# Optimization experiments

Measured on AMD Instinct MI355X. Metric: run time of the kernel, lower is better.

## Reference

```python
import jax, jax.numpy as jnp
import numpy as np

N = 50000       # nodes
E = 800000      # edges (avg degree 16)
R = 8           # relations
IN = 128        # in_channels
H = 128         # hidden_size
B = 10          # graphs in batch
NPG = N // B    # nodes per graph (equal-size graphs)
NEG_SLOPE = 0.2 # RGATConv default negative_slope


def setup_inputs() -> dict:
    key = jax.random.key(0)
    ks = jax.random.split(key, 12)
    s = 0.1
    x = jax.random.normal(ks[0], (N, IN), dtype=jnp.float32)
    edge_index = jax.random.randint(ks[1], (2, E), 0, N, dtype=jnp.int32)
    edge_type = jax.random.randint(ks[2], (E,), 0, R, dtype=jnp.int32)
    batch = jnp.repeat(jnp.arange(B, dtype=jnp.int32), NPG)
    W1 = jax.random.normal(ks[3], (R, IN, H), dtype=jnp.float32) * s
    q1 = jax.random.normal(ks[4], (H, 1), dtype=jnp.float32) * s
    k1 = jax.random.normal(ks[5], (H, 1), dtype=jnp.float32) * s
    b1 = jnp.zeros((H,), dtype=jnp.float32)
    W2 = jax.random.normal(ks[6], (R, H, H), dtype=jnp.float32) * s
    q2 = jax.random.normal(ks[7], (H, 1), dtype=jnp.float32) * s
    k2 = jax.random.normal(ks[8], (H, 1), dtype=jnp.float32) * s
    b2 = jnp.zeros((H,), dtype=jnp.float32)
    Wl = jax.random.normal(ks[9], (H, H), dtype=jnp.float32) * s
    bl = jnp.zeros((H,), dtype=jnp.float32)
    return dict(x=x, edge_index=edge_index, edge_type=edge_type, batch=batch,
                W1=W1, q1=q1, k1=k1, b1=b1, W2=W2, q2=q2, k2=k2, b2=b2,
                Wl=Wl, bl=bl)


def _rgat_conv(x, src, tgt, etype, W, q, k, b):
    # Per-relation transform once per node ([R,N,H]), then gather per edge;
    # mathematically identical to PyG's per-edge bmm but avoids the [E,in,H] blowup.
    xW = jnp.einsum('ni,rio->rno', x, W)          # [R, N, H]
    outi = xW[etype, tgt]                          # [E, H] transformed target feats
    outj = xW[etype, src]                          # [E, H] transformed source feats
    # additive self-attention, heads=1, dim=1
    alpha = jax.nn.leaky_relu(outi @ q + outj @ k, NEG_SLOPE)  # [E, 1]
    # across-relation segment softmax over incoming edges of each target node
    m = jax.ops.segment_max(alpha, tgt, num_segments=N)        # [N, 1]
    a = jnp.exp(alpha - m[tgt])
    den = jax.ops.segment_sum(a, tgt, num_segments=N)          # [N, 1]
    a = a / (den[tgt] + 1e-16)
    out = jax.ops.segment_sum(a * outj, tgt, num_segments=N)   # [N, H]
    return out + b


def reference(x, edge_index, edge_type, batch, W1, q1, k1, b1,
              W2, q2, k2, b2, Wl, bl):
    src, tgt = edge_index[0], edge_index[1]
    h = jax.nn.relu(_rgat_conv(x, src, tgt, edge_type, W1, q1, k1, b1))
    # dropout p=0 -> identity
    h = jax.nn.relu(_rgat_conv(h, src, tgt, edge_type, W2, q2, k2, b2))
    h = h @ Wl.T + bl                               # nn.Linear
    # to_dense_batch: batch is sorted with equal-size graphs of NPG nodes
    return h.reshape(B, NPG, H)
```

## Files before the change

kernel.cpp:

```cpp
#include <hip/hip_runtime.h>


typedef unsigned int uint;
typedef unsigned short ushort_t;

using bf16x8 = __attribute__((ext_vector_type(8))) __bf16;
using f32x4  = __attribute__((ext_vector_type(4))) float;

__device__ __forceinline__ ushort_t fToBf(float f) {
  uint u = __float_as_uint(f);
  u += 0x7FFFu + ((u >> 16) & 1);
  return (ushort_t)(u >> 16);
}
__device__ __forceinline__ float bfToF(ushort_t h) {
  return __uint_as_float(((uint)h) << 16);
}


__global__ void k_count(const int* __restrict__ tgt, int* __restrict__ deg, int E) {
  int e = blockIdx.x * 256 + threadIdx.x;
  if (e < E) atomicAdd(&deg[tgt[e]], 1);
}

__global__ void k_scanA(const int* __restrict__ deg, int* __restrict__ incl,
                        int* __restrict__ bsum, int n) {
  __shared__ int s[256];
  int tid = threadIdx.x;
  int i = blockIdx.x * 256 + tid;
  int v = (i < n) ? deg[i] : 0;
  s[tid] = v;
  __syncthreads();
  for (int off = 1; off < 256; off <<= 1) {
    int t = (tid >= off) ? s[tid - off] : 0;
    __syncthreads();
    s[tid] += t;
    __syncthreads();
  }
  if (i < n) incl[i] = s[tid];
  if (tid == 255) bsum[blockIdx.x] = s[255];
}

__global__ void k_scanB(int* __restrict__ bsum, int nb) {
  __shared__ int s[256];
  int tid = threadIdx.x;
  int v = (tid < nb) ? bsum[tid] : 0;
  s[tid] = v;
  __syncthreads();
  for (int off = 1; off < 256; off <<= 1) {
    int t = (tid >= off) ? s[tid - off] : 0;
    __syncthreads();
    s[tid] += t;
    __syncthreads();
  }
  if (tid < nb) bsum[tid] = s[tid] - v;
}

__global__ void k_scanC(const int* __restrict__ deg, const int* __restrict__ incl,
                        const int* __restrict__ bsum, int* __restrict__ rowptr,
                        int n, int E) {
  int i = blockIdx.x * 256 + threadIdx.x;
  if (i < n) {
    rowptr[i] = bsum[blockIdx.x] + incl[i] - deg[i];
    if (i == n - 1) rowptr[n] = E;
  }
}

__global__ void k_scatter(const int* __restrict__ src, const int* __restrict__ tgt,
                          const int* __restrict__ et, const int* __restrict__ rowptr,
                          int* __restrict__ cursor, int* __restrict__ sorted, int E) {
  int e = blockIdx.x * 256 + threadIdx.x;
  if (e >= E) return;
  int t = tgt[e];
  int pos = atomicAdd(&cursor[t], 1);
  sorted[rowptr[t] + pos] = src[e] | (et[e] << 16);
}


__global__ void k_wT(const float* __restrict__ W1, const float* __restrict__ W2,
                     ushort_t* __restrict__ WT) {
  int b = blockIdx.x;
  const float* W = (b >= 1024) ? W2 : W1;
  int rn = b & 1023;
  int r = rn >> 7, n = rn & 127;
  int k = threadIdx.x;
  WT[(size_t)b * 128 + k] = fToBf(W[((size_t)r * 128 + k) * 128 + n]);
}

__global__ void k_wqwk(const float* __restrict__ W1, const float* __restrict__ q1,
                       const float* __restrict__ k1, const float* __restrict__ W2,
                       const float* __restrict__ q2, const float* __restrict__ k2,
                       ushort_t* __restrict__ wqk) {
  int g = blockIdx.x * 256 + threadIdx.x;
  if (g >= 4096) return;
  int layer = g >> 11;
  int which = (g >> 10) & 1;
  int idx = g & 1023;
  const float* w = (layer ? W2 : W1) + (size_t)idx * 128;
  const float* v = layer ? (which ? k2 : q2) : (which ? k1 : q1);
  float s = 0.f;
  #pragma unroll 8
  for (int h = 0; h < 128; h++) s += w[h] * v[h];
  int r = idx >> 7, kin = idx & 127;
  wqk[(size_t)layer * 2048 + ((which << 3) + r) * 128 + kin] = fToBf(s);
}


#define LDA 136

template <bool F32IN>
__global__ __launch_bounds__(256, 3) void
k_gemm8(const void* __restrict__ Ain, const ushort_t* __restrict__ WT,
        const ushort_t* __restrict__ Wqk, ushort_t* __restrict__ xW,
        float* __restrict__ stbl, int M) {
  __shared__ ushort_t rp[4][32 * LDA];
  int tid = threadIdx.x, wv = tid >> 6, lane = tid & 63;
  int l15 = lane & 15, quad = lane >> 4;
  int node0 = blockIdx.x * 128 + wv * 32;
  ushort_t* rpw = rp[wv];

  bf16x8 bx[2][4];
  #pragma unroll
  for (int nt = 0; nt < 2; nt++) {
    int node = node0 + nt * 16 + l15;
    if (node >= M) node = M - 1;
    if (F32IN) {
      const float* row = (const float*)Ain + (size_t)node * 128;
      #pragma unroll
      for (int kb = 0; kb < 4; kb++) {
        float4 a = *(const float4*)(row + kb * 32 + quad * 8);
        float4 b = *(const float4*)(row + kb * 32 + quad * 8 + 4);
        union { bf16x8 v; ushort_t u[8]; } t;
        t.u[0] = fToBf(a.x); t.u[1] = fToBf(a.y); t.u[2] = fToBf(a.z); t.u[3] = fToBf(a.w);
        t.u[4] = fToBf(b.x); t.u[5] = fToBf(b.y); t.u[6] = fToBf(b.z); t.u[7] = fToBf(b.w);
        bx[nt][kb] = t.v;
      }
    } else {
      const ushort_t* row = (const ushort_t*)Ain + (size_t)node * 128;
      #pragma unroll
      for (int kb = 0; kb < 4; kb++)
        bx[nt][kb] = *(const bf16x8*)(row + kb * 32 + quad * 8);
    }
  }

  for (int r = 0; r < 8; r++) {
    const ushort_t* Wr = WT + (size_t)r * 16384;
    f32x4 acc0[8] = {}, acc1[8] = {};
    #pragma unroll
    for (int mt = 0; mt < 8; mt++) {
      bf16x8 af[4];
      #pragma unroll
      for (int kb = 0; kb < 4; kb++)
        af[kb] = *(const bf16x8*)(Wr + (size_t)(mt * 16 + l15) * 128 + kb * 32 + quad * 8);
      #pragma unroll
      for (int kb = 0; kb < 4; kb++) {
        acc0[mt] = __builtin_amdgcn_mfma_f32_16x16x32_bf16(af[kb], bx[0][kb], acc0[mt], 0, 0, 0);
        acc1[mt] = __builtin_amdgcn_mfma_f32_16x16x32_bf16(af[kb], bx[1][kb], acc1[mt], 0, 0, 0);
      }
    }
    #pragma unroll
    for (int mt = 0; mt < 8; mt++) {
      uint2 p0, p1;
      p0.x = (uint)fToBf(acc0[mt][0]) | ((uint)fToBf(acc0[mt][1]) << 16);
      p0.y = (uint)fToBf(acc0[mt][2]) | ((uint)fToBf(acc0[mt][3]) << 16);
      p1.x = (uint)fToBf(acc1[mt][0]) | ((uint)fToBf(acc1[mt][1]) << 16);
      p1.y = (uint)fToBf(acc1[mt][2]) | ((uint)fToBf(acc1[mt][3]) << 16);
      *(uint2*)(rpw + (size_t)l15 * LDA + mt * 16 + quad * 4) = p0;
      *(uint2*)(rpw + (size_t)(16 + l15) * LDA + mt * 16 + quad * 4) = p1;
    }
    #pragma unroll
    for (int i = 0; i < 8; i++) {
      int row = i * 4 + quad;
      int off = l15 * 8;
      int node = node0 + row;
      if (node < M) {
        int4 v = *(const int4*)(rpw + (size_t)row * LDA + off);
        *(int4*)(xW + ((size_t)r * M + node) * 128 + off) = v;
      }
    }
  }

  bf16x8 aq[4];
  #pragma unroll
  for (int kb = 0; kb < 4; kb++)
    aq[kb] = *(const bf16x8*)(Wqk + (size_t)l15 * 128 + kb * 32 + quad * 8);
  #pragma unroll
  for (int nt = 0; nt < 2; nt++) {
    f32x4 acc = {};
    #pragma unroll
    for (int kb = 0; kb < 4; kb++)
      acc = __builtin_amdgcn_mfma_f32_16x16x32_bf16(aq[kb], bx[nt][kb], acc, 0, 0, 0);
    int node = node0 + nt * 16 + l15;
    if (node < M) *(float4*)(stbl + (size_t)node * 16 + quad * 4) = *(float4*)&acc;
  }
}

__global__ __launch_bounds__(256) void
k_gemmL(const ushort_t* __restrict__ A, const float* __restrict__ Wl,
        float* __restrict__ Cout, const float* __restrict__ bias, int M) {
  __shared__ ushort_t As[64 * LDA];
  __shared__ ushort_t Bs[128 * LDA];
  int tid = threadIdx.x;
  int row0 = blockIdx.x * 64;
  for (int c = tid; c < 1024; c += 256) {
    int r = c >> 4, off = (c & 15) * 8;
    int4 v = {0, 0, 0, 0};
    if (row0 + r < M) v = *(const int4*)(A + (size_t)(row0 + r) * 128 + off);
    *(int4*)(As + r * LDA + off) = v;
  }
  for (int c = tid; c < 2048; c += 256) {
    int nn = c >> 4, off = (c & 15) * 8;
    float4 a = *(const float4*)(Wl + (size_t)nn * 128 + off);
    float4 b = *(const float4*)(Wl + (size_t)nn * 128 + off + 4);
    ushort_t* d = Bs + nn * LDA + off;
    d[0] = fToBf(a.x); d[1] = fToBf(a.y); d[2] = fToBf(a.z); d[3] = fToBf(a.w);
    d[4] = fToBf(b.x); d[5] = fToBf(b.y); d[6] = fToBf(b.z); d[7] = fToBf(b.w);
  }
  __syncthreads();
  int wv = tid >> 6, lane = tid & 63;
  int l15 = lane & 15, quad = lane >> 4;
  int wr = wv * 16;
  bf16x8 afr[4];
  #pragma unroll
  for (int kb = 0; kb < 4; kb++)
    afr[kb] = *reinterpret_cast<const bf16x8*>(As + (wr + l15) * LDA + kb * 32 + quad * 8);
  f32x4 acc[8] = {};
  #pragma unroll
  for (int ct = 0; ct < 8; ct++)
    #pragma unroll
    for (int kb = 0; kb < 4; kb++) {
      bf16x8 bfr = *reinterpret_cast<const bf16x8*>(Bs + (ct * 16 + l15) * LDA + kb * 32 + quad * 8);
      acc[ct] = __builtin_amdgcn_mfma_f32_16x16x32_bf16(afr[kb], bfr, acc[ct], 0, 0, 0);
    }
  #pragma unroll
  for (int ct = 0; ct < 8; ct++)
    #pragma unroll
    for (int reg = 0; reg < 4; reg++) {
      int rr = row0 + wr + quad * 4 + reg;
      if (rr < M) Cout[(size_t)rr * 128 + ct * 16 + l15] = acc[ct][reg] + bias[ct * 16 + l15];
    }
}


#define ACC8(W_, V_)                                                     \
  acc[0] += W_ * bfToF((ushort_t)(V_.x & 0xFFFF));                       \
  acc[1] += W_ * bfToF((ushort_t)(V_.x >> 16));                          \
  acc[2] += W_ * bfToF((ushort_t)(V_.y & 0xFFFF));                       \
  acc[3] += W_ * bfToF((ushort_t)(V_.y >> 16));                          \
  acc[4] += W_ * bfToF((ushort_t)(V_.z & 0xFFFF));                       \
  acc[5] += W_ * bfToF((ushort_t)(V_.z >> 16));                          \
  acc[6] += W_ * bfToF((ushort_t)(V_.w & 0xFFFF));                       \
  acc[7] += W_ * bfToF((ushort_t)(V_.w >> 16));

__global__ __launch_bounds__(256) void
k_aggr(const ushort_t* __restrict__ feat,
       const float* __restrict__ stbl,
       const int* __restrict__ rowptr, const int* __restrict__ sorted,
       const float* __restrict__ bias, ushort_t* __restrict__ outp, int n) {
  int tid = threadIdx.x, wv = tid >> 6, lane = tid & 63;
  int t = blockIdx.x * 4 + wv;
  if (t >= n) return;
  int e0 = rowptr[t], e1 = rowptr[t + 1];
  int g4 = lane >> 4, fcol = lane & 15;

  float m = -INFINITY, den = 0.f;
  float acc[8] = {};

  for (int base = e0; base < e1; base += 64) {
    int cnt = min(64, e1 - base);
    float alpha = -INFINITY;
    int pk = 0;
    if (lane < cnt) {
      pk = sorted[base + lane];
      int s = pk & 0xFFFF, r = pk >> 16;
      float a = stbl[(size_t)t * 16 + r] + stbl[(size_t)s * 16 + 8 + r];
      alpha = (a >= 0.f) ? a : 0.2f * a;
    }
    float cm = alpha;
    #pragma unroll
    for (int off = 32; off; off >>= 1) cm = fmaxf(cm, __shfl_xor(cm, off, 64));
    float nm = fmaxf(m, cm);
    float sc = __expf(m - nm);
    den *= sc;
    #pragma unroll
    for (int i = 0; i < 8; i++) acc[i] *= sc;
    float w = (lane < cnt) ? __expf(alpha - nm) : 0.f;
    float ws = w;
    #pragma unroll
    for (int off = 32; off; off >>= 1) ws += __shfl_xor(ws, off, 64);
    den += ws;
    m = nm;

    for (int g = 0; g < cnt; g += 16) {
      int i0 = g + g4;
      float w0 = __shfl(w, i0, 64);
      float w1 = __shfl(w, i0 + 4, 64);
      float w2 = __shfl(w, i0 + 8, 64);
      float w3 = __shfl(w, i0 + 12, 64);
      int p0 = __shfl(pk, i0, 64);
      int p1 = __shfl(pk, i0 + 4, 64);
      int p2 = __shfl(pk, i0 + 8, 64);
      int p3 = __shfl(pk, i0 + 12, 64);
      const uint4* r0 = (const uint4*)(feat + (size_t)((p0 >> 16) * n + (p0 & 0xFFFF)) * 128) + fcol;
      const uint4* r1 = (const uint4*)(feat + (size_t)((p1 >> 16) * n + (p1 & 0xFFFF)) * 128) + fcol;
      const uint4* r2 = (const uint4*)(feat + (size_t)((p2 >> 16) * n + (p2 & 0xFFFF)) * 128) + fcol;
      const uint4* r3 = (const uint4*)(feat + (size_t)((p3 >> 16) * n + (p3 & 0xFFFF)) * 128) + fcol;
      uint4 v0 = *r0;
      uint4 v1 = *r1;
      uint4 v2 = *r2;
      uint4 v3 = *r3;
      ACC8(w0, v0)
      ACC8(w1, v1)
      ACC8(w2, v2)
      ACC8(w3, v3)
    }
  }

  #pragma unroll
  for (int i = 0; i < 8; i++) acc[i] += __shfl_xor(acc[i], 16, 64);
  #pragma unroll
  for (int i = 0; i < 8; i++) acc[i] += __shfl_xor(acc[i], 32, 64);

  float inv = (den > 0.f) ? 1.f / (den + 1e-16f) : 0.f;
  uint4 o;
  uint* op = (uint*)&o;
  #pragma unroll
  for (int j = 0; j < 4; j++) {
    float a0 = fmaxf(acc[2 * j] * inv + bias[fcol * 8 + 2 * j], 0.f);
    float a1 = fmaxf(acc[2 * j + 1] * inv + bias[fcol * 8 + 2 * j + 1], 0.f);
    op[j] = (uint)fToBf(a0) | ((uint)fToBf(a1) << 16);
  }
  if (lane < 16) *(uint4*)(outp + (size_t)t * 128 + fcol * 8) = o;
}


extern "C" void kernel_launch(void* const* d_in, const int* in_sizes, int n_in,
                              void* d_out, int out_size, void* d_ws, size_t ws_size,
                              hipStream_t stream) {
  const float* x   = (const float*)d_in[0];
  const int* ei    = (const int*)d_in[1];
  const int* etype = (const int*)d_in[2];
  const float* W1  = (const float*)d_in[4];
  const float* q1  = (const float*)d_in[5];
  const float* k1  = (const float*)d_in[6];
  const float* b1  = (const float*)d_in[7];
  const float* W2  = (const float*)d_in[8];
  const float* q2  = (const float*)d_in[9];
  const float* k2  = (const float*)d_in[10];
  const float* b2  = (const float*)d_in[11];
  const float* Wl  = (const float*)d_in[12];
  const float* bl  = (const float*)d_in[13];
  float* out       = (float*)d_out;

  const int N = in_sizes[0] / 128;
  const int E = in_sizes[2];

  char* ws = (char*)d_ws;
  size_t off = 0;
  auto alloc = [&](size_t bytes) {
    size_t o = off;
    off = (off + bytes + 255) & ~(size_t)255;
    return o;
  };

  ushort_t* xW    = (ushort_t*)(ws + alloc((size_t)8 * N * 128 * 2));
  ushort_t* h1    = (ushort_t*)(ws + alloc((size_t)N * 128 * 2));
  ushort_t* h2    = (ushort_t*)(ws + alloc((size_t)N * 128 * 2));
  ushort_t* wT    = (ushort_t*)(ws + alloc((size_t)2 * 8 * 128 * 128 * 2));
  ushort_t* wqk   = (ushort_t*)(ws + alloc(2 * 16 * 128 * 2));
  float* stbl     = (float*)(ws + alloc((size_t)N * 16 * 4));
  int* deg        = (int*)(ws + alloc((size_t)N * 4));
  int* cursor     = (int*)(ws + alloc((size_t)N * 4));
  int* incl       = (int*)(ws + alloc((size_t)N * 4));
  int* rowptr     = (int*)(ws + alloc((size_t)(N + 1) * 4));
  int* bsum       = (int*)(ws + alloc(256 * 4));
  int* sorted     = (int*)(ws + alloc((size_t)E * 4));
  (void)ws_size; (void)n_in; (void)out_size;

  const int* srcp = ei;
  const int* tgtp = ei + E;

  int gE  = (E + 255) / 256;
  int gN  = (N + 255) / 256;
  int gW  = (N + 3) / 4;
  int gM  = (N + 63) / 64;
  int gM2 = (N + 127) / 128;

  hipMemsetAsync(deg, 0, (size_t)N * 4, stream);
  hipMemsetAsync(cursor, 0, (size_t)N * 4, stream);
  k_count<<<gE, 256, 0, stream>>>(tgtp, deg, E);
  k_scanA<<<gN, 256, 0, stream>>>(deg, incl, bsum, N);
  k_scanB<<<1, 256, 0, stream>>>(bsum, gN);
  k_scanC<<<gN, 256, 0, stream>>>(deg, incl, bsum, rowptr, N, E);
  k_scatter<<<gE, 256, 0, stream>>>(srcp, tgtp, etype, rowptr, cursor, sorted, E);

  k_wT<<<2048, 128, 0, stream>>>(W1, W2, wT);
  k_wqwk<<<16, 256, 0, stream>>>(W1, q1, k1, W2, q2, k2, wqk);

  k_gemm8<true><<<gM2, 256, 0, stream>>>(x, wT, wqk, xW, stbl, N);
  k_aggr<<<gW, 256, 0, stream>>>(xW, stbl, rowptr, sorted, b1, h1, N);

  k_gemm8<false><<<gM2, 256, 0, stream>>>(h1, wT + (size_t)8 * 128 * 128,
                                          wqk + 2048, xW, stbl, N);
  k_aggr<<<gW, 256, 0, stream>>>(xW, stbl, rowptr, sorted, b2, h2, N);

  k_gemmL<<<gM, 256, 0, stream>>>(h2, Wl, out, bl, N);
}
```

Baseline: 439.6 us.

## Split per-relation transform GEMM across a relation grid dimension with smaller node tiles

Replaces the per-block loop over all 8 relations with a 2D grid where blockIdx.y selects the relation, and shrinks each wave's tile from 32 to 16 nodes. This raises parallelism and occupancy (launch bounds go from 3 to 4 blocks) and cuts register and LDS use per block. In exchange, each input row is loaded and converted 8 times, once per relation. The attention-score table is computed only by the relation-0 blocks and now goes to a separate buffer per layer.

```diff
diff --git a/kernel.cpp b/kernel.cpp
--- a/kernel.cpp
+++ b/kernel.cpp
@@ -105,139 +105,83 @@
 }
 
 
-#define LDA 136
-
 template <bool F32IN>
-__global__ __launch_bounds__(256, 3) void
-k_gemm8(const void* __restrict__ Ain, const ushort_t* __restrict__ WT,
-        const ushort_t* __restrict__ Wqk, ushort_t* __restrict__ xW,
-        float* __restrict__ stbl, int M) {
-  __shared__ ushort_t rp[4][32 * LDA];
+__global__ __launch_bounds__(256, 4) void
+k_xw(const void* __restrict__ Ain,
+     const ushort_t* __restrict__ WT,
+     const ushort_t* __restrict__ Wqk,
+     ushort_t* __restrict__ xW,
+     float* __restrict__ stbl,
+     int M) {
+  __shared__ __align__(16) ushort_t rp[4][16 * 136];
   int tid = threadIdx.x, wv = tid >> 6, lane = tid & 63;
   int l15 = lane & 15, quad = lane >> 4;
-  int node0 = blockIdx.x * 128 + wv * 32;
+  int nodeBase = blockIdx.x * 64 + wv * 16;
+  int r = blockIdx.y;
   ushort_t* rpw = rp[wv];
 
-  bf16x8 bx[2][4];
-  #pragma unroll
-  for (int nt = 0; nt < 2; nt++) {
-    int node = node0 + nt * 16 + l15;
-    if (node >= M) node = M - 1;
-    if (F32IN) {
-      const float* row = (const float*)Ain + (size_t)node * 128;
-      #pragma unroll
-      for (int kb = 0; kb < 4; kb++) {
-        float4 a = *(const float4*)(row + kb * 32 + quad * 8);
-        float4 b = *(const float4*)(row + kb * 32 + quad * 8 + 4);
-        union { bf16x8 v; ushort_t u[8]; } t;
-        t.u[0] = fToBf(a.x); t.u[1] = fToBf(a.y); t.u[2] = fToBf(a.z); t.u[3] = fToBf(a.w);
-        t.u[4] = fToBf(b.x); t.u[5] = fToBf(b.y); t.u[6] = fToBf(b.z); t.u[7] = fToBf(b.w);
-        bx[nt][kb] = t.v;
-      }
-    } else {
-      const ushort_t* row = (const ushort_t*)Ain + (size_t)node * 128;
-      #pragma unroll
-      for (int kb = 0; kb < 4; kb++)
-        bx[nt][kb] = *(const bf16x8*)(row + kb * 32 + quad * 8);
-    }
-  }
-
-  for (int r = 0; r < 8; r++) {
-    const ushort_t* Wr = WT + (size_t)r * 16384;
-    f32x4 acc0[8] = {}, acc1[8] = {};
-    #pragma unroll
-    for (int mt = 0; mt < 8; mt++) {
-      bf16x8 af[4];
-      #pragma unroll
-      for (int kb = 0; kb < 4; kb++)
-        af[kb] = *(const bf16x8*)(Wr + (size_t)(mt * 16 + l15) * 128 + kb * 32 + quad * 8);
-      #pragma unroll
-      for (int kb = 0; kb < 4; kb++) {
-        acc0[mt] = __builtin_amdgcn_mfma_f32_16x16x32_bf16(af[kb], bx[0][kb], acc0[mt], 0, 0, 0);
-        acc1[mt] = __builtin_amdgcn_mfma_f32_16x16x32_bf16(af[kb], bx[1][kb], acc1[mt], 0, 0, 0);
-      }
-    }
-    #pragma unroll
-    for (int mt = 0; mt < 8; mt++) {
-      uint2 p0, p1;
-      p0.x = (uint)fToBf(acc0[mt][0]) | ((uint)fToBf(acc0[mt][1]) << 16);
-      p0.y = (uint)fToBf(acc0[mt][2]) | ((uint)fToBf(acc0[mt][3]) << 16);
-      p1.x = (uint)fToBf(acc1[mt][0]) | ((uint)fToBf(acc1[mt][1]) << 16);
-      p1.y = (uint)fToBf(acc1[mt][2]) | ((uint)fToBf(acc1[mt][3]) << 16);
-      *(uint2*)(rpw + (size_t)l15 * LDA + mt * 16 + quad * 4) = p0;
-      *(uint2*)(rpw + (size_t)(16 + l15) * LDA + mt * 16 + quad * 4) = p1;
-    }
-    #pragma unroll
-    for (int i = 0; i < 8; i++) {
-      int row = i * 4 + quad;
-      int off = l15 * 8;
-      int node = node0 + row;
-      if (node < M) {
-        int4 v = *(const int4*)(rpw + (size_t)row * LDA + off);
-        *(int4*)(xW + ((size_t)r * M + node) * 128 + off) = v;
-      }
-    }
-  }
-
-  bf16x8 aq[4];
-  #pragma unroll
-  for (int kb = 0; kb < 4; kb++)
-    aq[kb] = *(const bf16x8*)(Wqk + (size_t)l15 * 128 + kb * 32 + quad * 8);
-  #pragma unroll
-  for (int nt = 0; nt < 2; nt++) {
+  int node = nodeBase + l15;
+  int nc = node < M ? node : M - 1;
+
+  bf16x8 bx[4];
+  if (F32IN) {
+    const float* row = (const float*)Ain + (size_t)nc * 128;
+    #pragma unroll
+    for (int kb = 0; kb < 4; kb++) {
+      float4 a = *(const float4*)(row + kb * 32 + quad * 8);
+      float4 b = *(const float4*)(row + kb * 32 + quad * 8 + 4);
+      union { bf16x8 v; ushort_t u[8]; } t;
+      t.u[0] = fToBf(a.x); t.u[1] = fToBf(a.y); t.u[2] = fToBf(a.z); t.u[3] = fToBf(a.w);
+      t.u[4] = fToBf(b.x); t.u[5] = fToBf(b.y); t.u[6] = fToBf(b.z); t.u[7] = fToBf(b.w);
+      bx[kb] = t.v;
+    }
+  } else {
+    const ushort_t* row = (const ushort_t*)Ain + (size_t)nc * 128;
+    #pragma unroll
+    for (int kb = 0; kb < 4; kb++)
+      bx[kb] = *(const bf16x8*)(row + kb * 32 + quad * 8);
+  }
+
+  const ushort_t* Wr = WT + (size_t)r * 16384;
+  #pragma unroll
+  for (int mt = 0; mt < 8; mt++) {
+    bf16x8 af[4];
+    #pragma unroll
+    for (int kb = 0; kb < 4; kb++)
+      af[kb] = *(const bf16x8*)(Wr + (size_t)(mt * 16 + l15) * 128 + kb * 32 + quad * 8);
     f32x4 acc = {};
     #pragma unroll
     for (int kb = 0; kb < 4; kb++)
-      acc = __builtin_amdgcn_mfma_f32_16x16x32_bf16(aq[kb], bx[nt][kb], acc, 0, 0, 0);
-    int node = node0 + nt * 16 + l15;
-    if (node < M) *(float4*)(stbl + (size_t)node * 16 + quad * 4) = *(float4*)&acc;
-  }
-}
-
-__global__ __launch_bounds__(256) void
-k_gemmL(const ushort_t* __restrict__ A, const float* __restrict__ Wl,
-        float* __restrict__ Cout, const float* __restrict__ bias, int M) {
-  __shared__ ushort_t As[64 * LDA];
-  __shared__ ushort_t Bs[128 * LDA];
-  int tid = threadIdx.x;
-  int row0 = blockIdx.x * 64;
-  for (int c = tid; c < 1024; c += 256) {
-    int r = c >> 4, off = (c & 15) * 8;
-    int4 v = {0, 0, 0, 0};
-    if (row0 + r < M) v = *(const int4*)(A + (size_t)(row0 + r) * 128 + off);
-    *(int4*)(As + r * LDA + off) = v;
-  }
-  for (int c = tid; c < 2048; c += 256) {
-    int nn = c >> 4, off = (c & 15) * 8;
-    float4 a = *(const float4*)(Wl + (size_t)nn * 128 + off);
-    float4 b = *(const float4*)(Wl + (size_t)nn * 128 + off + 4);
-    ushort_t* d = Bs + nn * LDA + off;
-    d[0] = fToBf(a.x); d[1] = fToBf(a.y); d[2] = fToBf(a.z); d[3] = fToBf(a.w);
-    d[4] = fToBf(b.x); d[5] = fToBf(b.y); d[6] = fToBf(b.z); d[7] = fToBf(b.w);
-  }
-  __syncthreads();
-  int wv = tid >> 6, lane = tid & 63;
-  int l15 = lane & 15, quad = lane >> 4;
-  int wr = wv * 16;
-  bf16x8 afr[4];
-  #pragma unroll
-  for (int kb = 0; kb < 4; kb++)
-    afr[kb] = *reinterpret_cast<const bf16x8*>(As + (wr + l15) * LDA + kb * 32 + quad * 8);
-  f32x4 acc[8] = {};
-  #pragma unroll
-  for (int ct = 0; ct < 8; ct++)
-    #pragma unroll
-    for (int kb = 0; kb < 4; kb++) {
-      bf16x8 bfr = *reinterpret_cast<const bf16x8*>(Bs + (ct * 16 + l15) * LDA + kb * 32 + quad * 8);
-      acc[ct] = __builtin_amdgcn_mfma_f32_16x16x32_bf16(afr[kb], bfr, acc[ct], 0, 0, 0);
-    }
-  #pragma unroll
-  for (int ct = 0; ct < 8; ct++)
-    #pragma unroll
-    for (int reg = 0; reg < 4; reg++) {
-      int rr = row0 + wr + quad * 4 + reg;
-      if (rr < M) Cout[(size_t)rr * 128 + ct * 16 + l15] = acc[ct][reg] + bias[ct * 16 + l15];
-    }
+      acc = __builtin_amdgcn_mfma_f32_16x16x32_bf16(af[kb], bx[kb], acc, 0, 0, 0);
+    uint2 p;
+    p.x = (uint)fToBf(acc[0]) | ((uint)fToBf(acc[1]) << 16);
+    p.y = (uint)fToBf(acc[2]) | ((uint)fToBf(acc[3]) << 16);
+    *(uint2*)(rpw + (size_t)l15 * 136 + mt * 16 + quad * 4) = p;
+  }
+
+  if (blockIdx.y == 0) {
+    bf16x8 aq[4];
+    #pragma unroll
+    for (int kb = 0; kb < 4; kb++)
+      aq[kb] = *(const bf16x8*)(Wqk + (size_t)l15 * 128 + kb * 32 + quad * 8);
+    f32x4 s = {};
+    #pragma unroll
+    for (int kb = 0; kb < 4; kb++)
+      s = __builtin_amdgcn_mfma_f32_16x16x32_bf16(aq[kb], bx[kb], s, 0, 0, 0);
+    if (node < M) {
+      float4 v = {s[0], s[1], s[2], s[3]};
+      *(float4*)(stbl + (size_t)node * 16 + quad * 4) = v;
+    }
+  }
+
+  #pragma unroll
+  for (int k = 0; k < 4; k++) {
+    int row = k * 4 + quad;
+    int4 v = *(const int4*)(rpw + (size_t)row * 136 + l15 * 8);
+    int gn = nodeBase + row;
+    if (gn < M)
+      *(int4*)(xW + ((size_t)r * M + gn) * 128 + l15 * 8) = v;
+  }
 }
 
 
@@ -333,6 +277,55 @@
 }
 
 
+#define LDA 136
+
+__global__ __launch_bounds__(256) void
+k_gemmL(const ushort_t* __restrict__ A, const float* __restrict__ Wl,
+        float* __restrict__ Cout, const float* __restrict__ bias, int M) {
+  __shared__ ushort_t As[64 * LDA];
+  __shared__ ushort_t Bs[128 * LDA];
+  int tid = threadIdx.x;
+  int row0 = blockIdx.x * 64;
+  for (int c = tid; c < 1024; c += 256) {
+    int r = c >> 4, off = (c & 15) * 8;
+    int4 v = {0, 0, 0, 0};
+    if (row0 + r < M) v = *(const int4*)(A + (size_t)(row0 + r) * 128 + off);
+    *(int4*)(As + r * LDA + off) = v;
+  }
+  for (int c = tid; c < 2048; c += 256) {
+    int nn = c >> 4, off = (c & 15) * 8;
+    float4 a = *(const float4*)(Wl + (size_t)nn * 128 + off);
+    float4 b = *(const float4*)(Wl + (size_t)nn * 128 + off + 4);
+    ushort_t* d = Bs + nn * LDA + off;
+    d[0] = fToBf(a.x); d[1] = fToBf(a.y); d[2] = fToBf(a.z); d[3] = fToBf(a.w);
+    d[4] = fToBf(b.x); d[5] = fToBf(b.y); d[6] = fToBf(b.z); d[7] = fToBf(b.w);
+  }
+  __syncthreads();
+  int wv = tid >> 6, lane = tid & 63;
+  int l15 = lane & 15, quad = lane >> 4;
+  int wr = wv * 16;
+  bf16x8 afr[4];
+  #pragma unroll
+  for (int kb = 0; kb < 4; kb++)
+    afr[kb] = *reinterpret_cast<const bf16x8*>(As + (wr + l15) * LDA + kb * 32 + quad * 8);
+  f32x4 acc[8] = {};
+  #pragma unroll
+  for (int ct = 0; ct < 8; ct++)
+    #pragma unroll
+    for (int kb = 0; kb < 4; kb++) {
+      bf16x8 bfr = *reinterpret_cast<const bf16x8*>(Bs + (ct * 16 + l15) * LDA + kb * 32 + quad * 8);
+      acc[ct] = __builtin_amdgcn_mfma_f32_16x16x32_bf16(afr[kb], bfr, acc[ct], 0, 0, 0);
+    }
+  #pragma unroll
+  for (int ct = 0; ct < 8; ct++)
+    #pragma unroll
+    for (int reg = 0; reg < 4; reg++) {
+      int rr = row0 + wr + quad * 4 + reg;
+      if (rr < M) Cout[(size_t)rr * 128 + ct * 16 + l15] = acc[ct][reg] + bias[ct * 16 + l15];
+    }
+}
+
+
 extern "C" void kernel_launch(void* const* d_in, const int* in_sizes, int n_in,
                               void* d_out, int out_size, void* d_ws, size_t ws_size,
                               hipStream_t stream) {
@@ -367,7 +360,8 @@
   ushort_t* h2    = (ushort_t*)(ws + alloc((size_t)N * 128 * 2));
   ushort_t* wT    = (ushort_t*)(ws + alloc((size_t)2 * 8 * 128 * 128 * 2));
   ushort_t* wqk   = (ushort_t*)(ws + alloc(2 * 16 * 128 * 2));
-  float* stbl     = (float*)(ws + alloc((size_t)N * 16 * 4));
+  float* stblA    = (float*)(ws + alloc((size_t)N * 16 * 4));
+  float* stblB    = (float*)(ws + alloc((size_t)N * 16 * 4));
   int* deg        = (int*)(ws + alloc((size_t)N * 4));
   int* cursor     = (int*)(ws + alloc((size_t)N * 4));
   int* incl       = (int*)(ws + alloc((size_t)N * 4));
@@ -379,11 +373,10 @@
   const int* srcp = ei;
   const int* tgtp = ei + E;
 
-  int gE  = (E + 255) / 256;
-  int gN  = (N + 255) / 256;
-  int gW  = (N + 3) / 4;
-  int gM  = (N + 63) / 64;
-  int gM2 = (N + 127) / 128;
+  int gE = (E + 255) / 256;
+  int gN = (N + 255) / 256;
+  int gW = (N + 3) / 4;
+  int gX = (N + 63) / 64;
 
   hipMemsetAsync(deg, 0, (size_t)N * 4, stream);
   hipMemsetAsync(cursor, 0, (size_t)N * 4, stream);
@@ -396,12 +389,12 @@
   k_wT<<<2048, 128, 0, stream>>>(W1, W2, wT);
   k_wqwk<<<16, 256, 0, stream>>>(W1, q1, k1, W2, q2, k2, wqk);
 
-  k_gemm8<true><<<gM2, 256, 0, stream>>>(x, wT, wqk, xW, stbl, N);
-  k_aggr<<<gW, 256, 0, stream>>>(xW, stbl, rowptr, sorted, b1, h1, N);
-
-  k_gemm8<false><<<gM2, 256, 0, stream>>>(h1, wT + (size_t)8 * 128 * 128,
-                                          wqk + 2048, xW, stbl, N);
-  k_aggr<<<gW, 256, 0, stream>>>(xW, stbl, rowptr, sorted, b2, h2, N);
-
-  k_gemmL<<<gM, 256, 0, stream>>>(h2, Wl, out, bl, N);
-}
+  k_xw<true><<<dim3(gX, 8), 256, 0, stream>>>(x, wT, wqk, xW, stblA, N);
+  k_aggr<<<gW, 256, 0, stream>>>(xW, stblA, rowptr, sorted, b1, h1, N);
+
+  k_xw<false><<<dim3(gX, 8), 256, 0, stream>>>(h1, wT + (size_t)8 * 128 * 128,
+                                               wqk + 2048, xW, stblB, N);
+  k_aggr<<<gW, 256, 0, stream>>>(xW, stblB, rowptr, sorted, b2, h2, N);
+
+  k_gemmL<<<gX, 256, 0, stream>>>(h2, Wl, out, bl, N);
+}
```

Measured after the change: 536.3 us. +22.0%, slower.
